# Performance work log

Measured on AMD Instinct MI355X. Metric: run time of the kernel, lower is better.

Reference implementation:

```python
import jax, jax.numpy as jnp
import numpy as np

NSAMPLE = 1024   # npoint (FPS centroids)
NGROUP = 32      # K neighbors per centroid
BN_EPS = 1e-5
MLP_DIMS = [(67, 64), (64, 64), (64, 128)]


def setup_inputs() -> dict:
    key = jax.random.key(0)
    ks = jax.random.split(key, 2 + len(MLP_DIMS))
    B, N, D = 16, 4096, 64
    inp = {
        "xyz": jax.random.normal(ks[0], (B, N, 3), jnp.float32),
        "points_fea": jax.random.normal(ks[1], (B, N, D), jnp.float32),
    }
    for i, (cin, cout) in enumerate(MLP_DIMS):
        inp[f"W{i}"] = jax.random.normal(ks[2 + i], (cout, cin), jnp.float32) / np.float32(np.sqrt(cin))
        inp[f"b{i}"] = jnp.zeros((cout,), jnp.float32)
        inp[f"g{i}"] = jnp.ones((cout,), jnp.float32)
        inp[f"beta{i}"] = jnp.zeros((cout,), jnp.float32)
    return inp


def _fps(xyz, npoint):
    """Farthest point sampling. xyz [B,N,3] -> idx [B,npoint] int32.
    Uses squared distances (same argmin/argmax ordering as euclidean)."""
    B, N, _ = xyz.shape

    def step(carry, _):
        dist, far = carry                                   # [B,N], [B]
        c = jnp.take_along_axis(xyz, far[:, None, None], axis=1)  # [B,1,3]
        d = jnp.sum((xyz - c) ** 2, axis=-1)                # [B,N]
        dist = jnp.minimum(dist, d)
        return (dist, jnp.argmax(dist, axis=-1).astype(jnp.int32)), far

    init = (jnp.full((B, N), 1e10, jnp.float32), jnp.zeros((B,), jnp.int32))
    _, idx = jax.lax.scan(step, init, None, length=npoint)  # [npoint,B]
    return idx.T


def _knn_idx(q, p, k):
    """k nearest neighbors of q [B,S,3] among p [B,N,3] -> idx [B,S,k]."""
    d = (jnp.sum(q * q, -1)[:, :, None] + jnp.sum(p * p, -1)[:, None, :]
         - 2.0 * jnp.einsum('bsc,bnc->bsn', q, p))
    _, idx = jax.lax.top_k(-d, k)
    return idx


def _gather(points, idx):
    """points [B,N,C], idx [B,S,K] -> [B,S,K,C]."""
    B, S, K = idx.shape
    flat = jnp.take_along_axis(points, idx.reshape(B, S * K)[..., None], axis=1)
    return flat.reshape(B, S, K, points.shape[-1])


def reference(xyz, points_fea, W0, b0, g0, beta0, W1, b1, g1, beta1, W2, b2, g2, beta2):
    fps_idx = _fps(xyz, NSAMPLE)
    sampled_xyz = jnp.take_along_axis(xyz, fps_idx[..., None], axis=1)      # [B,S,3]
    gidx = _knn_idx(sampled_xyz, xyz, NGROUP)                               # [B,S,K]
    gxyz = _gather(xyz, gidx) - sampled_xyz[:, :, None, :]                  # [B,S,K,3]
    gfeat = _gather(points_fea, gidx)                                       # [B,S,K,D]
    x = jnp.concatenate([gxyz, gfeat], axis=-1)                             # [B,S,K,3+D]

    # shared MLP: 1x1 conv == per-point linear; BN (training stats) over B,S,K per channel
    for W, b, g, be in ((W0, b0, g0, beta0), (W1, b1, g1, beta1), (W2, b2, g2, beta2)):
        x = jnp.einsum('bskc,oc->bsko', x, W) + b
        mu = jnp.mean(x, axis=(0, 1, 2))
        var = jnp.var(x, axis=(0, 1, 2))
        x = jax.nn.relu((x - mu) * jax.lax.rsqrt(var + BN_EPS) * g + be)

    feats = jnp.max(x, axis=2)                                              # [B,S,Cout]
    return sampled_xyz, feats
```

## Files before the change

### kernel.cpp

```cpp
#include <hip/hip_runtime.h>
#include <cstdint>
#include <cstddef>

typedef unsigned short ushort_t;
typedef unsigned int uint_t;
typedef unsigned long long u64_t;
typedef float v2f __attribute__((ext_vector_type(2)));

#define B_ 16
#define N_ 4096
#define S_ 1024
#define K_ 32
#define NR 524288
#define NQ 16384

__device__ __forceinline__ float bf2f(ushort_t u) {
    union { uint_t i; float f; } x; x.i = ((uint_t)u) << 16; return x.f;
}
__device__ __forceinline__ ushort_t f2bf(float f) {
    union { float f; uint_t u; } x; x.f = f;
    uint_t u = x.u;
    uint_t r = (u + 0x7fffu + ((u >> 16) & 1u)) >> 16;
    return (ushort_t)r;
}

template <int CTRL>
__device__ __forceinline__ uint_t dppmov(uint_t v, uint_t idt) {
    return (uint_t)__builtin_amdgcn_update_dpp((int)idt, (int)v, CTRL, 0xF, 0xF, false);
}

__device__ __forceinline__ void wave_argmax64(uint_t& hi, uint_t& lo) {
#define STEP_MAX(C) { uint_t nh = dppmov<C>(hi, 0u); uint_t nl = dppmov<C>(lo, 0u); \
    u64_t a = ((u64_t)hi << 32) | lo, bb = ((u64_t)nh << 32) | nl; \
    if (bb > a) { hi = nh; lo = nl; } }
    STEP_MAX(0x111) STEP_MAX(0x112) STEP_MAX(0x114) STEP_MAX(0x118)
    STEP_MAX(0x142) STEP_MAX(0x143)
#undef STEP_MAX
}

__device__ __forceinline__ void wave_argmin64(uint_t& hi, uint_t& lo) {
#define STEP_MIN(C) { uint_t nh = dppmov<C>(hi, 0xFFFFFFFFu); uint_t nl = dppmov<C>(lo, 0xFFFFFFFFu); \
    u64_t a = ((u64_t)hi << 32) | lo, bb = ((u64_t)nh << 32) | nl; \
    if (bb < a) { hi = nh; lo = nl; } }
    STEP_MIN(0x111) STEP_MIN(0x112) STEP_MIN(0x114) STEP_MIN(0x118)
    STEP_MIN(0x142) STEP_MIN(0x143)
#undef STEP_MIN
}

__global__ __launch_bounds__(256) void prep_kernel(
        const float* __restrict__ W0, const float* __restrict__ W1,
        const float* __restrict__ W2,
        float* __restrict__ wt0, float* __restrict__ wt1, float* __restrict__ wt2) {
    int tid = threadIdx.x;
    for (int i = tid; i < 64 * 67; i += 256) { int o = i / 67, c = i % 67; wt0[c * 64 + o] = W0[i]; }
    for (int i = tid; i < 64 * 64; i += 256) { int o = i >> 6, c = i & 63; wt1[c * 64 + o] = W1[i]; }
    for (int i = tid; i < 128 * 64; i += 256) { int o = i >> 6, c = i & 63; wt2[c * 128 + o] = W2[i]; }
}

__global__ __launch_bounds__(256) void fps_kernel(
        const float* __restrict__ xyz, float* __restrict__ out_sxyz) {
    #pragma clang fp contract(off)
    __shared__ float4 pts[N_];
    __shared__ uint2 cand[2][4];
    int b = blockIdx.x, tid = threadIdx.x;
    int wv = tid >> 6, lane = tid & 63;
    const float* base = xyz + (size_t)b * N_ * 3;

    v2f px[8], py[8], pz[8], dist[8];
    #pragma unroll
    for (int t = 0; t < 16; t++) {
        int p = tid + t * 256;
        float x = base[p * 3 + 0];
        float y = base[p * 3 + 1];
        float z = base[p * 3 + 2];
        px[t >> 1][t & 1] = x; py[t >> 1][t & 1] = y; pz[t >> 1][t & 1] = z;
        pts[p] = make_float4(x, y, z, 0.0f);
        dist[t >> 1][t & 1] = 1e10f;
    }
    __syncthreads();

    int far = 0;
    for (int i = 0; i < S_; i++) {
        float4 c = pts[far];
        if (tid == 0) {
            int qi = b * S_ + i;
            out_sxyz[qi * 3 + 0] = c.x;
            out_sxyz[qi * 3 + 1] = c.y;
            out_sxyz[qi * 3 + 2] = c.z;
        }
        v2f cx = { c.x, c.x }, cy = { c.y, c.y }, cz = { c.z, c.z };
        #pragma unroll
        for (int j = 0; j < 8; j++) {
            v2f dx = px[j] - cx, dy = py[j] - cy, dz = pz[j] - cz;
            v2f d = (dx * dx + dy * dy) + dz * dz;
            dist[j] = __builtin_elementwise_min(dist[j], d);
        }
        uint_t kh[16], kl[16];
        #pragma unroll
        for (int t = 0; t < 16; t++) {
            kh[t] = __float_as_uint(dist[t >> 1][t & 1]);
            kl[t] = ~(uint_t)(tid + t * 256);
        }
        #pragma unroll
        for (int st = 8; st >= 1; st >>= 1) {
            #pragma unroll
            for (int t = 0; t < 8; t++) {
                if (t < st) {
                    u64_t a = ((u64_t)kh[t] << 32) | kl[t];
                    u64_t bb = ((u64_t)kh[t + st] << 32) | kl[t + st];
                    if (bb > a) { kh[t] = kh[t + st]; kl[t] = kl[t + st]; }
                }
            }
        }
        uint_t bh = kh[0], bl = kl[0];
        wave_argmax64(bh, bl);
        int buf = i & 1;
        if (lane == 63) cand[buf][wv] = make_uint2(bh, bl);
        __syncthreads();
        uint2 c0 = cand[buf][0], c1 = cand[buf][1], c2 = cand[buf][2], c3 = cand[buf][3];
        u64_t best = ((u64_t)c0.x << 32) | c0.y;
        u64_t k1 = ((u64_t)c1.x << 32) | c1.y; if (k1 > best) best = k1;
        u64_t k2 = ((u64_t)c2.x << 32) | c2.y; if (k2 > best) best = k2;
        u64_t k3 = ((u64_t)c3.x << 32) | c3.y; if (k3 > best) best = k3;
        far = (int)((~(uint_t)best) & 4095u);
    }
}

__global__ __launch_bounds__(64) void knn_kernel(
        const float* __restrict__ xyz, const float* __restrict__ qxyz,
        int* __restrict__ nbr) {
    #pragma clang fp contract(off)
    __shared__ uint_t dsm[N_];
    int bs = blockIdx.x;
    int b = bs >> 10;
    int lane = threadIdx.x;
    const float* xb = xyz + (size_t)b * N_ * 3;

    float qx = qxyz[bs * 3 + 0], qy = qxyz[bs * 3 + 1], qz = qxyz[bs * 3 + 2];
    float qq = (qx * qx + qy * qy) + qz * qz;

    uint_t ulv = 0xFFFFFFFFu; int li = 0;
    for (int s = 0; s < 64; s++) {
        int p = s * 64 + lane;
        float x = xb[p * 3 + 0];
        float y = xb[p * 3 + 1];
        float z = xb[p * 3 + 2];
        float pp = (x * x + y * y) + z * z;
        float dt = (qx * x + qy * y) + qz * z;
        float d = (qq + pp) - 2.0f * dt;
        uint_t ub = __float_as_uint(d);
        ub ^= (uint_t)(((int)ub >> 31)) | 0x80000000u;
        dsm[s * 64 + ((lane + s) & 63)] = ub;
        if (ub < ulv) { ulv = ub; li = p; }
    }
    __syncthreads();

    u64_t mask = 0ull;
    int my_nbr = 0;
    for (int r = 0; r < K_; r++) {
        uint_t hh = ulv, ll = (uint_t)li;
        wave_argmin64(hh, ll);
        int idx = (int)(uint_t)__builtin_amdgcn_readlane((int)ll, 63);
        int glane = idx & 63, srow = idx >> 6;
        if (lane == r) my_nbr = idx;
        if (lane == glane) mask |= 1ull << srow;
        uint_t gml = (uint_t)__builtin_amdgcn_readlane((int)(uint_t)mask, glane);
        uint_t gmh = (uint_t)__builtin_amdgcn_readlane((int)(uint_t)(mask >> 32), glane);
        u64_t gm = ((u64_t)gmh << 32) | gml;
        uint_t cv = ((gm >> lane) & 1ull) ? 0xFFFFFFFFu
                                          : dsm[lane * 64 + ((glane + lane) & 63)];
        uint_t ci = (uint_t)(lane * 64 + glane);
        wave_argmin64(cv, ci);
        uint_t rv = (uint_t)__builtin_amdgcn_readlane((int)cv, 63);
        uint_t ri = (uint_t)__builtin_amdgcn_readlane((int)ci, 63);
        if (lane == glane) { ulv = rv; li = (int)ri; }
    }
    if (lane < K_) nbr[bs * K_ + lane] = my_nbr;
}

__global__ __launch_bounds__(256) void l0_kernel(
        const float* __restrict__ xyz, const float* __restrict__ fea,
        const float* __restrict__ qxyz, const int* __restrict__ nbr,
        const float* __restrict__ wt0, ushort_t* __restrict__ yT) {
    int row = blockIdx.x * 256 + threadIdx.x;
    int bs = row >> 5, b = bs >> 10;
    int p = nbr[row];
    p = (p < 0) ? 0 : (p > N_ - 1 ? N_ - 1 : p);
    float qx = qxyz[bs * 3 + 0], qy = qxyz[bs * 3 + 1], qz = qxyz[bs * 3 + 2];
    const float* xb = xyz + ((size_t)b * N_ + p) * 3;
    float dx = xb[0] - qx, dy = xb[1] - qy, dz = xb[2] - qz;

    float acc[64];
    #pragma unroll
    for (int o = 0; o < 64; o++)
        acc[o] = fmaf(dz, wt0[128 + o], fmaf(dy, wt0[64 + o], dx * wt0[o]));

    const float4* fr = (const float4*)(fea + ((size_t)b * N_ + p) * 64);
    #pragma unroll 2
    for (int i = 0; i < 16; i++) {
        float4 u = fr[i];
        float ua[4] = { u.x, u.y, u.z, u.w };
        #pragma unroll
        for (int j = 0; j < 4; j++) {
            const float* w = wt0 + (3 + i * 4 + j) * 64;
            #pragma unroll
            for (int o = 0; o < 64; o++) acc[o] = fmaf(ua[j], w[o], acc[o]);
        }
    }
    #pragma unroll
    for (int o = 0; o < 64; o++)
        yT[(size_t)o * NR + row] = f2bf(acc[o]);
}

__global__ __launch_bounds__(256) void stats_pass(
        const ushort_t* __restrict__ y, float* __restrict__ part) {
    int cb = blockIdx.x;
    int c = cb >> 5, ch = cb & 31;
    const uint4* src = (const uint4*)(y + (size_t)c * NR + (size_t)ch * 16384);
    float s = 0.0f, q = 0.0f;
    for (int i = threadIdx.x; i < 2048; i += 256) {
        uint4 u = src[i];
        uint_t ua[4] = { u.x, u.y, u.z, u.w };
        #pragma unroll
        for (int j = 0; j < 4; j++) {
            float v0 = bf2f((ushort_t)(ua[j] & 0xffffu));
            float v1 = bf2f((ushort_t)(ua[j] >> 16));
            s += v0; q = fmaf(v0, v0, q);
            s += v1; q = fmaf(v1, v1, q);
        }
    }
    __shared__ float ls[256], lq[256];
    int tid = threadIdx.x;
    ls[tid] = s; lq[tid] = q;
    __syncthreads();
    for (int off = 128; off >= 1; off >>= 1) {
        if (tid < off) { ls[tid] += ls[tid + off]; lq[tid] += lq[tid + off]; }
        __syncthreads();
    }
    if (tid == 0) { part[cb * 2 + 0] = ls[0]; part[cb * 2 + 1] = lq[0]; }
}

__global__ __launch_bounds__(64) void stats_fin(
        const float* __restrict__ part, const float* __restrict__ g,
        const float* __restrict__ be, float* __restrict__ ab) {
    int o = threadIdx.x;
    double s = 0.0, q = 0.0;
    for (int ch = 0; ch < 32; ch++) {
        s += (double)part[(o * 32 + ch) * 2 + 0];
        q += (double)part[(o * 32 + ch) * 2 + 1];
    }
    double mu = s / (double)NR;
    double var = q / (double)NR - mu * mu;
    if (var < 0.0) var = 0.0;
    double a = (double)g[o] / sqrt(var + 1e-5);
    ab[o]      = (float)a;
    ab[64 + o] = (float)((double)be[o] - mu * a);
}

__global__ __launch_bounds__(256) void l1_kernel(
        ushort_t* yT, const float* __restrict__ wt1, const float* __restrict__ ab) {
    int row = blockIdx.x * 256 + threadIdx.x;
    float xv[64];
    #pragma unroll
    for (int c = 0; c < 64; c++)
        xv[c] = fmaxf(fmaf(bf2f(yT[(size_t)c * NR + row]), ab[c], ab[64 + c]), 0.0f);
    float acc[64];
    #pragma unroll
    for (int o = 0; o < 64; o++) acc[o] = 0.0f;
    #pragma unroll 4
    for (int c = 0; c < 64; c++) {
        const float* w = wt1 + c * 64;
        #pragma unroll
        for (int o = 0; o < 64; o++) acc[o] = fmaf(xv[c], w[o], acc[o]);
    }
    #pragma unroll
    for (int o = 0; o < 64; o++)
        yT[(size_t)o * NR + row] = f2bf(acc[o]);
}

__global__ __launch_bounds__(256) void l2s_kernel(
        const ushort_t* __restrict__ yT, const float* __restrict__ wt2,
        const float* __restrict__ ab1, float* __restrict__ part2s,
        float* __restrict__ M) {
    int bx = blockIdx.x, half = blockIdx.y;
    int tid = threadIdx.x;
    int row = bx * 256 + tid;
    int lane = tid & 63, wv = tid >> 6;
    float xv[64];
    #pragma unroll
    for (int c = 0; c < 64; c++)
        xv[c] = fmaxf(fmaf(bf2f(yT[(size_t)c * NR + row]), ab1[c], ab1[64 + c]), 0.0f);
    float acc[64];
    #pragma unroll
    for (int o = 0; o < 64; o++) acc[o] = 0.0f;
    const float* w = wt2 + half * 64;
    #pragma unroll 4
    for (int c = 0; c < 64; c++) {
        const float* wr = w + c * 128;
        #pragma unroll
        for (int o = 0; o < 64; o++) acc[o] = fmaf(xv[c], wr[o], acc[o]);
    }
    __shared__ float Msm[4][2][64];
    __shared__ float Ssm[4][64], Qsm[4][64];
    #pragma unroll 2
    for (int o = 0; o < 64; o++) {
        float v = acc[o];
        float m = v;
        #pragma unroll
        for (int mo = 1; mo <= 16; mo <<= 1) m = fmaxf(m, __shfl_xor(m, mo));
        float s = v, q = v * v;
        #pragma unroll
        for (int mo = 1; mo <= 32; mo <<= 1) { s += __shfl_xor(s, mo); q += __shfl_xor(q, mo); }
        if (lane == 0)  { Msm[wv][0][o] = m; Ssm[wv][o] = s; Qsm[wv][o] = q; }
        if (lane == 32) { Msm[wv][1][o] = m; }
    }
    __syncthreads();
    #pragma unroll
    for (int r = 0; r < 2; r++) {
        int e = tid + r * 256;
        int ewv = e >> 7, eq = (e >> 6) & 1, eo = e & 63;
        M[(size_t)(bx * 8 + ewv * 2 + eq) * 128 + half * 64 + eo] = Msm[ewv][eq][eo];
    }
    if (tid < 64) {
        float s = Ssm[0][tid] + Ssm[1][tid] + Ssm[2][tid] + Ssm[3][tid];
        part2s[(size_t)(half * 64 + tid) * 2048 + bx] = s;
    } else if (tid < 128) {
        int ch = tid - 64;
        float q = Qsm[0][ch] + Qsm[1][ch] + Qsm[2][ch] + Qsm[3][ch];
        part2s[(size_t)128 * 2048 + (size_t)(half * 64 + ch) * 2048 + bx] = q;
    }
}

__global__ __launch_bounds__(256) void stats2_fin(
        const float* __restrict__ part2s, const float* __restrict__ g,
        const float* __restrict__ be, float* __restrict__ ab2) {
    int og = blockIdx.x;
    float s = 0.0f, q = 0.0f;
    for (int col = threadIdx.x; col < 2048; col += 256) {
        s += part2s[(size_t)og * 2048 + col];
        q += part2s[(size_t)128 * 2048 + (size_t)og * 2048 + col];
    }
    __shared__ float ls[256], lq[256];
    int tid = threadIdx.x;
    ls[tid] = s; lq[tid] = q;
    __syncthreads();
    for (int off = 128; off >= 1; off >>= 1) {
        if (tid < off) { ls[tid] += ls[tid + off]; lq[tid] += lq[tid + off]; }
        __syncthreads();
    }
    if (tid == 0) {
        double mu = (double)ls[0] / (double)NR;
        double var = (double)lq[0] / (double)NR - mu * mu;
        if (var < 0.0) var = 0.0;
        double a = (double)g[og] / sqrt(var + 1e-5);
        ab2[og]       = (float)a;
        ab2[128 + og] = (float)((double)be[og] - mu * a);
    }
}

__global__ __launch_bounds__(256) void fin_kernel(
        const float* __restrict__ M, const float* __restrict__ ab2,
        float* __restrict__ out) {
    int idx = blockIdx.x * 256 + threadIdx.x;
    int og = idx & 127;
    out[49152 + idx] = fmaxf(fmaf(M[idx], ab2[og], ab2[128 + og]), 0.0f);
}

extern "C" void kernel_launch(void* const* d_in, const int* in_sizes, int n_in,
                              void* d_out, int out_size, void* d_ws, size_t ws_size,
                              hipStream_t stream) {
    const float* xyz = (const float*)d_in[0];
    const float* fea = (const float*)d_in[1];
    const float* W0  = (const float*)d_in[2];
    const float* g0  = (const float*)d_in[4];
    const float* be0 = (const float*)d_in[5];
    const float* W1  = (const float*)d_in[6];
    const float* g1  = (const float*)d_in[8];
    const float* be1 = (const float*)d_in[9];
    const float* W2  = (const float*)d_in[10];
    const float* g2  = (const float*)d_in[12];
    const float* be2 = (const float*)d_in[13];
    float* out = (float*)d_out;

    char* w = (char*)d_ws;
    ushort_t* yT    = (ushort_t*)(w);
    int*      nbr   = (int*)     (w + 67108864);
    float*    part2s= (float*)   (w + 67108864);
    float*    part  = (float*)   (w + 69206016);
    float*    M     = (float*)   (w + 69222400);
    float*    ab0   = (float*)   (w + 77611008);
    float*    ab1   = (float*)   (w + 77611520);
    float*    ab2   = (float*)   (w + 77612032);
    float*    wt0   = (float*)   (w + 77613056);
    float*    wt1   = (float*)   (w + 77630208);
    float*    wt2   = (float*)   (w + 77646592);

    prep_kernel<<<1, 256, 0, stream>>>(W0, W1, W2, wt0, wt1, wt2);
    fps_kernel<<<B_, 256, 0, stream>>>(xyz, out);
    knn_kernel<<<NQ, 64, 0, stream>>>(xyz, out, nbr);

    l0_kernel<<<2048, 256, 0, stream>>>(xyz, fea, out, nbr, wt0, yT);
    stats_pass<<<64 * 32, 256, 0, stream>>>(yT, part);
    stats_fin<<<1, 64, 0, stream>>>(part, g0, be0, ab0);

    l1_kernel<<<2048, 256, 0, stream>>>(yT, wt1, ab0);
    stats_pass<<<64 * 32, 256, 0, stream>>>(yT, part);
    stats_fin<<<1, 64, 0, stream>>>(part, g1, be1, ab1);

    l2s_kernel<<<dim3(2048, 2), 256, 0, stream>>>(yT, wt2, ab1, part2s, M);
    stats2_fin<<<128, 256, 0, stream>>>(part2s, g2, be2, ab2);
    fin_kernel<<<8192, 256, 0, stream>>>(M, ab2, out);
}
```

Measured before the change: 1.408 ms.

## Fuse BN statistics into layer kernels with DPP reductions, defer FPS output writes

The separate stats_pass kernels, which re-read the bf16 activations after layers 0 and 1, are removed. Each layer kernel now computes per-block channel sums and sums of squares with DPP wave reductions and writes partials that a 64-block stats_fin reduces. The l2s reduction switches from shuffles to DPP, and FPS records indices in shared memory and writes sampled coordinates after the loop instead of once per iteration. This saves two full passes over the activation buffer but adds reduction work inside the layer kernels, and the final statistics sum order changes from double to float accumulation.

```diff
diff --git a/kernel.cpp b/kernel.cpp
--- a/kernel.cpp
+++ b/kernel.cpp
@@ -27,6 +27,14 @@
 template <int CTRL>
 __device__ __forceinline__ uint_t dppmov(uint_t v, uint_t idt) {
     return (uint_t)__builtin_amdgcn_update_dpp((int)idt, (int)v, CTRL, 0xF, 0xF, false);
+}
+template <int CTRL>
+__device__ __forceinline__ float dppsum(float v) {
+    return v + __uint_as_float(dppmov<CTRL>(__float_as_uint(v), 0u));
+}
+template <int CTRL>
+__device__ __forceinline__ float dppmaxf(float v) {
+    return fmaxf(v, __uint_as_float(dppmov<CTRL>(__float_as_uint(v), 0xFF800000u)));
 }
 
 __device__ __forceinline__ void wave_argmax64(uint_t& hi, uint_t& lo) {
@@ -37,7 +45,6 @@
     STEP_MAX(0x142) STEP_MAX(0x143)
 #undef STEP_MAX
 }
-
 __device__ __forceinline__ void wave_argmin64(uint_t& hi, uint_t& lo) {
 #define STEP_MIN(C) { uint_t nh = dppmov<C>(hi, 0xFFFFFFFFu); uint_t nl = dppmov<C>(lo, 0xFFFFFFFFu); \
     u64_t a = ((u64_t)hi << 32) | lo, bb = ((u64_t)nh << 32) | nl; \
@@ -62,6 +69,7 @@
     #pragma clang fp contract(off)
     __shared__ float4 pts[N_];
     __shared__ uint2 cand[2][4];
+    __shared__ int farh[S_];
     int b = blockIdx.x, tid = threadIdx.x;
     int wv = tid >> 6, lane = tid & 63;
     const float* base = xyz + (size_t)b * N_ * 3;
@@ -82,12 +90,7 @@
     int far = 0;
     for (int i = 0; i < S_; i++) {
         float4 c = pts[far];
-        if (tid == 0) {
-            int qi = b * S_ + i;
-            out_sxyz[qi * 3 + 0] = c.x;
-            out_sxyz[qi * 3 + 1] = c.y;
-            out_sxyz[qi * 3 + 2] = c.z;
-        }
+        if (tid == 0) farh[i] = far;
         v2f cx = { c.x, c.x }, cy = { c.y, c.y }, cz = { c.z, c.z };
         #pragma unroll
         for (int j = 0; j < 8; j++) {
@@ -124,6 +127,14 @@
         u64_t k3 = ((u64_t)c3.x << 32) | c3.y; if (k3 > best) best = k3;
         far = (int)((~(uint_t)best) & 4095u);
     }
+    __syncthreads();
+    for (int i = tid; i < S_; i += 256) {
+        float4 c = pts[farh[i]];
+        int qi = b * S_ + i;
+        out_sxyz[qi * 3 + 0] = c.x;
+        out_sxyz[qi * 3 + 1] = c.y;
+        out_sxyz[qi * 3 + 2] = c.z;
+    }
 }
 
 __global__ __launch_bounds__(64) void knn_kernel(
@@ -181,8 +192,11 @@
 __global__ __launch_bounds__(256) void l0_kernel(
         const float* __restrict__ xyz, const float* __restrict__ fea,
         const float* __restrict__ qxyz, const int* __restrict__ nbr,
-        const float* __restrict__ wt0, ushort_t* __restrict__ yT) {
-    int row = blockIdx.x * 256 + threadIdx.x;
+        const float* __restrict__ wt0, ushort_t* __restrict__ yT,
+        float* __restrict__ MPart) {
+    int bx = blockIdx.x, tid = threadIdx.x;
+    int row = bx * 256 + tid;
+    int lane = tid & 63, wv = tid >> 6;
     int bs = row >> 5, b = bs >> 10;
     int p = nbr[row];
     p = (p < 0) ? 0 : (p > N_ - 1 ? N_ - 1 : p);
@@ -207,27 +221,36 @@
             for (int o = 0; o < 64; o++) acc[o] = fmaf(ua[j], w[o], acc[o]);
         }
     }
-    #pragma unroll
-    for (int o = 0; o < 64; o++)
-        yT[(size_t)o * NR + row] = f2bf(acc[o]);
-}
-
-__global__ __launch_bounds__(256) void stats_pass(
-        const ushort_t* __restrict__ y, float* __restrict__ part) {
-    int cb = blockIdx.x;
-    int c = cb >> 5, ch = cb & 31;
-    const uint4* src = (const uint4*)(y + (size_t)c * NR + (size_t)ch * 16384);
+    __shared__ float Ssm[4][64], Qsm[4][64];
+    #pragma unroll 4
+    for (int o = 0; o < 64; o++) {
+        ushort_t hb = f2bf(acc[o]);
+        yT[(size_t)o * NR + row] = hb;
+        float v = bf2f(hb);
+        float s = v, q = v * v;
+        s = dppsum<0x111>(s); s = dppsum<0x112>(s); s = dppsum<0x114>(s);
+        s = dppsum<0x118>(s); s = dppsum<0x142>(s); s = dppsum<0x143>(s);
+        q = dppsum<0x111>(q); q = dppsum<0x112>(q); q = dppsum<0x114>(q);
+        q = dppsum<0x118>(q); q = dppsum<0x142>(q); q = dppsum<0x143>(q);
+        if (lane == 63) { Ssm[wv][o] = s; Qsm[wv][o] = q; }
+    }
+    __syncthreads();
+    if (tid < 64)
+        MPart[bx * 128 + tid] = Ssm[0][tid] + Ssm[1][tid] + Ssm[2][tid] + Ssm[3][tid];
+    else if (tid < 128) {
+        int ch = tid - 64;
+        MPart[bx * 128 + tid] = Qsm[0][ch] + Qsm[1][ch] + Qsm[2][ch] + Qsm[3][ch];
+    }
+}
+
+__global__ __launch_bounds__(256) void stats_fin(
+        const float* __restrict__ MPart, const float* __restrict__ g,
+        const float* __restrict__ be, float* __restrict__ ab) {
+    int o = blockIdx.x;
     float s = 0.0f, q = 0.0f;
-    for (int i = threadIdx.x; i < 2048; i += 256) {
-        uint4 u = src[i];
-        uint_t ua[4] = { u.x, u.y, u.z, u.w };
-        #pragma unroll
-        for (int j = 0; j < 4; j++) {
-            float v0 = bf2f((ushort_t)(ua[j] & 0xffffu));
-            float v1 = bf2f((ushort_t)(ua[j] >> 16));
-            s += v0; q = fmaf(v0, v0, q);
-            s += v1; q = fmaf(v1, v1, q);
-        }
+    for (int col = threadIdx.x; col < 2048; col += 256) {
+        s += MPart[col * 128 + o];
+        q += MPart[col * 128 + 64 + o];
     }
     __shared__ float ls[256], lq[256];
     int tid = threadIdx.x;
@@ -237,29 +260,22 @@
         if (tid < off) { ls[tid] += ls[tid + off]; lq[tid] += lq[tid + off]; }
         __syncthreads();
     }
-    if (tid == 0) { part[cb * 2 + 0] = ls[0]; part[cb * 2 + 1] = lq[0]; }
-}
-
-__global__ __launch_bounds__(64) void stats_fin(
-        const float* __restrict__ part, const float* __restrict__ g,
-        const float* __restrict__ be, float* __restrict__ ab) {
-    int o = threadIdx.x;
-    double s = 0.0, q = 0.0;
-    for (int ch = 0; ch < 32; ch++) {
-        s += (double)part[(o * 32 + ch) * 2 + 0];
-        q += (double)part[(o * 32 + ch) * 2 + 1];
-    }
-    double mu = s / (double)NR;
-    double var = q / (double)NR - mu * mu;
-    if (var < 0.0) var = 0.0;
-    double a = (double)g[o] / sqrt(var + 1e-5);
-    ab[o]      = (float)a;
-    ab[64 + o] = (float)((double)be[o] - mu * a);
+    if (tid == 0) {
+        double mu = (double)ls[0] / (double)NR;
+        double var = (double)lq[0] / (double)NR - mu * mu;
+        if (var < 0.0) var = 0.0;
+        double a = (double)g[o] / sqrt(var + 1e-5);
+        ab[o]      = (float)a;
+        ab[64 + o] = (float)((double)be[o] - mu * a);
+    }
 }
 
 __global__ __launch_bounds__(256) void l1_kernel(
-        ushort_t* yT, const float* __restrict__ wt1, const float* __restrict__ ab) {
-    int row = blockIdx.x * 256 + threadIdx.x;
+        ushort_t* yT, const float* __restrict__ wt1, const float* __restrict__ ab,
+        float* __restrict__ MPart) {
+    int bx = blockIdx.x, tid = threadIdx.x;
+    int row = bx * 256 + tid;
+    int lane = tid & 63, wv = tid >> 6;
     float xv[64];
     #pragma unroll
     for (int c = 0; c < 64; c++)
@@ -273,9 +289,26 @@
         #pragma unroll
         for (int o = 0; o < 64; o++) acc[o] = fmaf(xv[c], w[o], acc[o]);
     }
-    #pragma unroll
-    for (int o = 0; o < 64; o++)
-        yT[(size_t)o * NR + row] = f2bf(acc[o]);
+    __shared__ float Ssm[4][64], Qsm[4][64];
+    #pragma unroll 4
+    for (int o = 0; o < 64; o++) {
+        ushort_t hb = f2bf(acc[o]);
+        yT[(size_t)o * NR + row] = hb;
+        float v = bf2f(hb);
+        float s = v, q = v * v;
+        s = dppsum<0x111>(s); s = dppsum<0x112>(s); s = dppsum<0x114>(s);
+        s = dppsum<0x118>(s); s = dppsum<0x142>(s); s = dppsum<0x143>(s);
+        q = dppsum<0x111>(q); q = dppsum<0x112>(q); q = dppsum<0x114>(q);
+        q = dppsum<0x118>(q); q = dppsum<0x142>(q); q = dppsum<0x143>(q);
+        if (lane == 63) { Ssm[wv][o] = s; Qsm[wv][o] = q; }
+    }
+    __syncthreads();
+    if (tid < 64)
+        MPart[bx * 128 + tid] = Ssm[0][tid] + Ssm[1][tid] + Ssm[2][tid] + Ssm[3][tid];
+    else if (tid < 128) {
+        int ch = tid - 64;
+        MPart[bx * 128 + tid] = Qsm[0][ch] + Qsm[1][ch] + Qsm[2][ch] + Qsm[3][ch];
+    }
 }
 
 __global__ __launch_bounds__(256) void l2s_kernel(
@@ -302,17 +335,19 @@
     }
     __shared__ float Msm[4][2][64];
     __shared__ float Ssm[4][64], Qsm[4][64];
-    #pragma unroll 2
+    #pragma unroll 4
     for (int o = 0; o < 64; o++) {
         float v = acc[o];
         float m = v;
-        #pragma unroll
-        for (int mo = 1; mo <= 16; mo <<= 1) m = fmaxf(m, __shfl_xor(m, mo));
+        m = dppmaxf<0x111>(m); m = dppmaxf<0x112>(m); m = dppmaxf<0x114>(m);
+        m = dppmaxf<0x118>(m); m = dppmaxf<0x142>(m);
         float s = v, q = v * v;
-        #pragma unroll
-        for (int mo = 1; mo <= 32; mo <<= 1) { s += __shfl_xor(s, mo); q += __shfl_xor(q, mo); }
-        if (lane == 0)  { Msm[wv][0][o] = m; Ssm[wv][o] = s; Qsm[wv][o] = q; }
-        if (lane == 32) { Msm[wv][1][o] = m; }
+        s = dppsum<0x111>(s); s = dppsum<0x112>(s); s = dppsum<0x114>(s);
+        s = dppsum<0x118>(s); s = dppsum<0x142>(s); s = dppsum<0x143>(s);
+        q = dppsum<0x111>(q); q = dppsum<0x112>(q); q = dppsum<0x114>(q);
+        q = dppsum<0x118>(q); q = dppsum<0x142>(q); q = dppsum<0x143>(q);
+        if (lane == 31) Msm[wv][0][o] = m;
+        if (lane == 63) { Msm[wv][1][o] = m; Ssm[wv][o] = s; Qsm[wv][o] = q; }
     }
     __syncthreads();
     #pragma unroll
@@ -386,8 +421,8 @@
     ushort_t* yT    = (ushort_t*)(w);
     int*      nbr   = (int*)     (w + 67108864);
     float*    part2s= (float*)   (w + 67108864);
-    float*    part  = (float*)   (w + 69206016);
     float*    M     = (float*)   (w + 69222400);
+    float*    MPart = (float*)   (w + 69222400);
     float*    ab0   = (float*)   (w + 77611008);
     float*    ab1   = (float*)   (w + 77611520);
     float*    ab2   = (float*)   (w + 77612032);
@@ -399,13 +434,11 @@
     fps_kernel<<<B_, 256, 0, stream>>>(xyz, out);
     knn_kernel<<<NQ, 64, 0, stream>>>(xyz, out, nbr);
 
-    l0_kernel<<<2048, 256, 0, stream>>>(xyz, fea, out, nbr, wt0, yT);
-    stats_pass<<<64 * 32, 256, 0, stream>>>(yT, part);
-    stats_fin<<<1, 64, 0, stream>>>(part, g0, be0, ab0);
-
-    l1_kernel<<<2048, 256, 0, stream>>>(yT, wt1, ab0);
-    stats_pass<<<64 * 32, 256, 0, stream>>>(yT, part);
-    stats_fin<<<1, 64, 0, stream>>>(part, g1, be1, ab1);
+    l0_kernel<<<2048, 256, 0, stream>>>(xyz, fea, out, nbr, wt0, yT, MPart);
+    stats_fin<<<64, 256, 0, stream>>>(MPart, g0, be0, ab0);
+
+    l1_kernel<<<2048, 256, 0, stream>>>(yT, wt1, ab0, MPart);
+    stats_fin<<<64, 256, 0, stream>>>(MPart, g1, be1, ab1);
 
     l2s_kernel<<<dim3(2048, 2), 256, 0, stream>>>(yT, wt2, ab1, part2s, M);
     stats2_fin<<<128, 256, 0, stream>>>(part2s, g2, be2, ab2);
```

Result: slower. 1.761 ms (+25.0%).
